# Kernel tuning notes

Measured on AMD Instinct MI355X. Metric: run time of the kernel, lower is better.

## Reference

```python
import jax, jax.numpy as jnp
import numpy as np

K = 9          # knn_num
EPS = 1e-5     # BatchNorm eps


def _conv2d(x, w, stride):
    # x: NCHW, w: OIHW, VALID padding
    return jax.lax.conv_general_dilated(
        x, w, window_strides=stride, padding='VALID',
        dimension_numbers=('NCHW', 'OIHW', 'NCHW'))


def _bn_relu(x, gamma, beta):
    # training-mode BatchNorm2d (biased batch stats over N,H,W) + ReLU
    mean = jnp.mean(x, axis=(0, 2, 3), keepdims=True)
    var = jnp.var(x, axis=(0, 2, 3), keepdims=True)
    xhat = (x - mean) * jax.lax.rsqrt(var + EPS)
    return jax.nn.relu(xhat * gamma[None, :, None, None] + beta[None, :, None, None])


def setup_inputs() -> dict:
    key = jax.random.key(0)
    ks = jax.random.split(key, 5)
    B, C, N = 16, 128, 2048
    features = jax.random.normal(ks[0], (B, C, N, 1), dtype=jnp.float32)
    fan1 = 2 * C * 1 * 3
    W1 = jax.random.normal(ks[1], (C, 2 * C, 1, 3), dtype=jnp.float32) / np.sqrt(fan1)
    b1 = jnp.zeros((C,), dtype=jnp.float32)
    g1 = jnp.ones((C,), dtype=jnp.float32)
    beta1 = jnp.zeros((C,), dtype=jnp.float32)
    fan2 = C * 1 * 3
    W2 = jax.random.normal(ks[2], (C, C, 1, 3), dtype=jnp.float32) / np.sqrt(fan2)
    b2 = jnp.zeros((C,), dtype=jnp.float32)
    g2 = jnp.ones((C,), dtype=jnp.float32)
    beta2 = jnp.zeros((C,), dtype=jnp.float32)
    return {"features": features, "W1": W1, "b1": b1, "g1": g1, "beta1": beta1,
            "W2": W2, "b2": b2, "g2": g2, "beta2": beta2}


def reference(features, W1, b1, g1, beta1, W2, b2, g2, beta2):
    B, C, N, _ = features.shape
    x = features.reshape(B, C, N)
    # pairwise_distance[b,i,j] = -||x_i||^2 + 2 x_i.x_j - ||x_j||^2 = -||x_i - x_j||^2
    xx = jnp.sum(x * x, axis=1)                      # (B, N)
    inner = jnp.einsum('bci,bcj->bij', x, x)          # (B, N, N)
    pd = 2.0 * inner - xx[:, :, None] - xx[:, None, :]
    _, idx = jax.lax.top_k(pd, K)                     # (B, N, K) nearest neighbors (incl. self)
    xT = jnp.transpose(x, (0, 2, 1))                  # (B, N, C)
    feature = xT[jnp.arange(B)[:, None, None], idx]   # (B, N, K, C) gathered neighbors
    xc = xT[:, :, None, :]                            # (B, N, 1, C)
    diff = xc - feature
    # torch: cat(x, (x - f) - |x - f|) along channel dim -> (B, N, K, 2C)
    edge = jnp.concatenate(
        [jnp.broadcast_to(xc, diff.shape), diff - jnp.abs(diff)], axis=3)
    edge = jnp.transpose(edge, (0, 3, 1, 2))          # (B, 2C, N, K)
    h = _conv2d(edge, W1, (1, 3)) + b1[None, :, None, None]   # (B, C, N, 3)
    h = _bn_relu(h, g1, beta1)
    h = _conv2d(h, W2, (1, 1)) + b2[None, :, None, None]       # (B, C, N, 1)
    h = _bn_relu(h, g2, beta2)
    return h
```

## Files before the change

### kernel.cpp

```cpp
#include <hip/hip_runtime.h>
#include <cstddef>

#define BATCH 16
#define CH    128
#define NPTS  2048
#define KNN   9

typedef const __attribute__((address_space(1))) void* gptr_t;
typedef __attribute__((address_space(3))) void* lptr_t;

__global__ void k_transpose(const float* __restrict__ x, float* __restrict__ xT) {
  __shared__ float tile[32][33];
  int b = blockIdx.z;
  int n0 = blockIdx.x * 32, c0 = blockIdx.y * 32;
  int tx = threadIdx.x, ty = threadIdx.y;
#pragma unroll
  for (int i = 0; i < 4; ++i) {
    int cc = c0 + ty + i * 8;
    tile[ty + i * 8][tx] = x[((size_t)b * CH + cc) * NPTS + n0 + tx];
  }
  __syncthreads();
#pragma unroll
  for (int i = 0; i < 4; ++i) {
    int nn = n0 + ty + i * 8;
    xT[((size_t)b * NPTS + nn) * CH + c0 + tx] = tile[tx][ty + i * 8];
  }
}

__global__ void k_xx_pw(const float* __restrict__ x, float* __restrict__ xx) {
  int g = blockIdx.x * 256 + threadIdx.x;
  int b = g >> 11, n = g & (NPTS - 1);
  const float* p = x + (size_t)b * CH * NPTS + n;
  float s[128];
#pragma unroll
  for (int c = 0; c < 128; ++c) {
    float v = p[(size_t)c * NPTS];
    s[c] = __fmul_rn(v, v);
  }
  float lane[16];
#pragma unroll
  for (int l = 0; l < 16; ++l) {
    lane[l] = __fadd_rn(
        __fadd_rn(__fadd_rn(s[l], s[16 + l]), __fadd_rn(s[32 + l], s[48 + l])),
        __fadd_rn(__fadd_rn(s[64 + l], s[80 + l]), __fadd_rn(s[96 + l], s[112 + l])));
  }
  float m8[8];
#pragma unroll
  for (int i = 0; i < 8; ++i) m8[i] = __fadd_rn(lane[i], lane[i + 8]);
  float n4[4];
#pragma unroll
  for (int i = 0; i < 4; ++i) n4[i] = __fadd_rn(m8[i], m8[i + 4]);
  float p2[2];
#pragma unroll
  for (int i = 0; i < 2; ++i) p2[i] = __fadd_rn(n4[i], n4[i + 2]);
  xx[g] = __fadd_rn(p2[0], p2[1]);
}

__global__ __launch_bounds__(256) void k_knn_np(const float* __restrict__ x,
                                                const float* __restrict__ xx,
                                                int* __restrict__ idxout) {
  __shared__ __align__(16) char smraw[65536];
  float (*rowT)[64] = (float (*)[64])smraw;
  float* colA = (float*)(smraw + 32768);
  float* colB = (float*)(smraw + 49152);
  float (*mv)[145] = (float (*)[145])smraw;
  unsigned short (*mi)[145] = (unsigned short (*)[145])(smraw + 37120);

  int b = blockIdx.y;
  int n0 = blockIdx.x * 64;
  int tid = threadIdx.x;
  int tx = tid & 15, ty = tid >> 4;

  const float* gb = x + (size_t)b * CH * NPTS;

#pragma unroll
  for (int i = 0; i < 8; ++i) {
    int e = i * 1024 + tid * 4;
    const float* ga = gb + (size_t)(e >> 6) * NPTS + n0 + (e & 63);
    __builtin_amdgcn_global_load_lds((gptr_t)ga, (lptr_t)(&rowT[0][0] + e), 16, 0, 0);
  }

  float tv[4][9];
  int   ti[4][9];
#pragma unroll
  for (int m = 0; m < 4; ++m)
#pragma unroll
    for (int s = 0; s < 9; ++s) { tv[m][s] = -3.4e38f; ti[m][s] = 0x7fffffff; }

  float xr[4];
#pragma unroll
  for (int m = 0; m < 4; ++m) xr[m] = xx[(size_t)b * NPTS + n0 + ty * 4 + m];

#pragma unroll
  for (int i = 0; i < 4; ++i) {
    int e = i * 1024 + tid * 4;
    const float* ga = gb + (size_t)(e >> 6) * NPTS + 0 + (e & 63);
    __builtin_amdgcn_global_load_lds((gptr_t)ga, (lptr_t)(colA + e), 16, 0, 0);
  }

  for (int jt = 0; jt < NPTS; jt += 64) {
    int jnext = (jt + 64) & (NPTS - 1);

    __builtin_amdgcn_s_barrier();
#pragma unroll
    for (int i = 0; i < 4; ++i) {
      int e = i * 1024 + tid * 4;
      const float* ga = gb + (size_t)(64 + (e >> 6)) * NPTS + jt + (e & 63);
      __builtin_amdgcn_global_load_lds((gptr_t)ga, (lptr_t)(colB + e), 16, 0, 0);
    }
    asm volatile("s_waitcnt vmcnt(4)" ::: "memory");
    __builtin_amdgcn_s_barrier();

    float acc[4][4];
#pragma unroll
    for (int m = 0; m < 4; ++m)
#pragma unroll
      for (int nn = 0; nn < 4; ++nn) acc[m][nn] = 0.f;

#pragma unroll 8
    for (int k2 = 0; k2 < 64; ++k2) {
      float a[4], bv[4];
      *(float4*)a  = *(const float4*)&rowT[k2][ty * 4];
      *(float4*)bv = *(const float4*)(colA + k2 * 64 + tx * 4);
#pragma unroll
      for (int m = 0; m < 4; ++m)
#pragma unroll
        for (int nn = 0; nn < 4; ++nn)
          acc[m][nn] = __builtin_fmaf(a[m], bv[nn], acc[m][nn]);
    }

    __builtin_amdgcn_s_barrier();
#pragma unroll
    for (int i = 0; i < 4; ++i) {
      int e = i * 1024 + tid * 4;
      const float* ga = gb + (size_t)(e >> 6) * NPTS + jnext + (e & 63);
      __builtin_amdgcn_global_load_lds((gptr_t)ga, (lptr_t)(colA + e), 16, 0, 0);
    }
    asm volatile("s_waitcnt vmcnt(4)" ::: "memory");
    __builtin_amdgcn_s_barrier();

#pragma unroll 8
    for (int k2 = 0; k2 < 64; ++k2) {
      float a[4], bv[4];
      *(float4*)a  = *(const float4*)&rowT[64 + k2][ty * 4];
      *(float4*)bv = *(const float4*)(colB + k2 * 64 + tx * 4);
#pragma unroll
      for (int m = 0; m < 4; ++m)
#pragma unroll
        for (int nn = 0; nn < 4; ++nn)
          acc[m][nn] = __builtin_fmaf(a[m], bv[nn], acc[m][nn]);
    }

#pragma unroll
    for (int nn = 0; nn < 4; ++nn) {
      int j = jt + tx * 4 + nn;
      float xc = xx[(size_t)b * NPTS + j];
#pragma unroll
      for (int m = 0; m < 4; ++m) {
        float val = __fsub_rn(__fsub_rn(__fmul_rn(2.0f, acc[m][nn]), xr[m]), xc);
        if (val > tv[m][8]) {
          float cv = val; int ci = j;
#pragma unroll
          for (int s = 0; s < 9; ++s) {
            bool sw = cv > tv[m][s];
            float t1 = tv[m][s]; int t2 = ti[m][s];
            tv[m][s] = sw ? cv : t1;  ti[m][s] = sw ? ci : t2;
            cv = sw ? t1 : cv;        ci = sw ? t2 : ci;
          }
        }
      }
    }
  }

  __syncthreads();
#pragma unroll
  for (int m = 0; m < 4; ++m) {
    int row = ty * 4 + m;
#pragma unroll
    for (int s = 0; s < 9; ++s) {
      mv[row][tx * 9 + s] = tv[m][s];
      mi[row][tx * 9 + s] = (unsigned short)ti[m][s];
    }
  }
  __syncthreads();
  if (tid < 64) {
    int row = tid;
    size_t base = ((size_t)b * NPTS + n0 + row) * KNN;
    for (int s = 0; s < KNN; ++s) {
      float best = -3.4e38f; int bj = 0x7fffffff; int bq = 0;
      for (int q = 0; q < 144; ++q) {
        float v = mv[row][q]; int jj = (int)mi[row][q];
        if (v > best || (v == best && jj < bj)) { best = v; bj = jj; bq = q; }
      }
      mv[row][bq] = -3.4e38f;
      idxout[base + s] = bj;
    }
  }
}

__global__ void k_prep(const float* __restrict__ W1, const float* __restrict__ W2,
                       float* __restrict__ At, float* __restrict__ W2t) {
  int g = blockIdx.x * 256 + threadIdx.x;
  if (g < 512 * 128) {
    int k = g / 128, o = g % 128;
    float v;
    if (k < 384) v = W1[(size_t)o * 768 + 384 + k];
    else {
      int c = k - 384;
      v = W1[(size_t)o * 768 + c * 3] + W1[(size_t)o * 768 + c * 3 + 1] +
          W1[(size_t)o * 768 + c * 3 + 2];
    }
    At[(size_t)k * 128 + o] = v;
  }
  if (g < 384 * 128) {
    int k = g / 128, o = g % 128;
    W2t[(size_t)k * 128 + o] = W2[(size_t)o * 384 + k];
  }
}

#define NN1 8
__global__ __launch_bounds__(256) void k_conv1(const float* __restrict__ xT,
                                               const int* __restrict__ knn_idx,
                                               const float* __restrict__ At,
                                               const float* __restrict__ bias1,
                                               float* __restrict__ h1) {
  __shared__ float dminL[NN1][KNN][132];
  __shared__ float xnL[NN1][132];
  __shared__ __align__(16) float AL[32][128];
  __shared__ int   idxL[NN1][KNN];
  int b = blockIdx.y;
  int n0 = blockIdx.x * NN1;
  int tid = threadIdx.x;

  if (tid < NN1 * KNN) {
    int n = tid / KNN, k = tid % KNN;
    idxL[n][k] = knn_idx[((size_t)b * NPTS + n0 + n) * KNN + k];
  }
  {
    int n = tid >> 5, q = tid & 31;
    float4 v = *(const float4*)&xT[((size_t)b * NPTS + n0 + n) * CH + q * 4];
    *(float4*)&xnL[n][q * 4] = v;
  }
  __syncthreads();
#pragma unroll
  for (int i = 0; i < 9; ++i) {
    int e = tid + i * 256;
    int rrow = e >> 5, q = e & 31;
    int n = rrow / KNN, k = rrow % KNN;
    int j = idxL[n][k];
    float4 xj = *(const float4*)&xT[((size_t)b * NPTS + j) * CH + q * 4];
    float4 xn = *(const float4*)&xnL[n][q * 4];
    float4 d;
    d.x = 2.0f * fminf(xn.x - xj.x, 0.0f);
    d.y = 2.0f * fminf(xn.y - xj.y, 0.0f);
    d.z = 2.0f * fminf(xn.z - xj.z, 0.0f);
    d.w = 2.0f * fminf(xn.w - xj.w, 0.0f);
    *(float4*)&dminL[n][k][q * 4] = d;
  }

  int n = tid & (NN1 - 1);
  int og = tid >> 3;
  float acc[4][3];
#pragma unroll
  for (int o = 0; o < 4; ++o)
#pragma unroll
    for (int t = 0; t < 3; ++t) acc[o][t] = 0.f;

  for (int kc = 0; kc < 16; ++kc) {
    __syncthreads();
#pragma unroll
    for (int i = 0; i < 3; ++i) {
      int e = i * 1024 + tid * 4;
      const float* ga = At + (size_t)kc * 3072 + e;
      __builtin_amdgcn_global_load_lds((gptr_t)ga, (lptr_t)(&AL[0][0] + e), 16, 0, 0);
    }
    asm volatile("s_waitcnt vmcnt(0)" ::: "memory");
    __syncthreads();

#pragma unroll
    for (int half = 0; half < 2; ++half) {
      int cbase = kc * 8 + half * 4;
      float q9[9][4];
#pragma unroll
      for (int nr = 0; nr < 9; ++nr)
        *(float4*)q9[nr] = *(const float4*)&dminL[n][nr][cbase];

#pragma unroll
      for (int kk = 0; kk < 12; ++kk) {
        int ci = kk / 3, r = kk % 3;
        float a[4];
        *(float4*)a = *(const float4*)&AL[half * 12 + kk][og * 4];
#pragma unroll
        for (int o = 0; o < 4; ++o) {
          acc[o][0] = fmaf(a[o], q9[r][ci],     acc[o][0]);
          acc[o][1] = fmaf(a[o], q9[3 + r][ci], acc[o][1]);
          acc[o][2] = fmaf(a[o], q9[6 + r][ci], acc[o][2]);
        }
      }
    }
  }

  for (int kc2 = 0; kc2 < 4; ++kc2) {
    __syncthreads();
#pragma unroll
    for (int i = 0; i < 4; ++i) {
      int e = i * 1024 + tid * 4;
      const float* ga = At + (size_t)(384 + kc2 * 32) * 128 + e;
      __builtin_amdgcn_global_load_lds((gptr_t)ga, (lptr_t)(&AL[0][0] + e), 16, 0, 0);
    }
    asm volatile("s_waitcnt vmcnt(0)" ::: "memory");
    __syncthreads();
#pragma unroll 4
    for (int kk = 0; kk < 32; ++kk) {
      int c = kc2 * 32 + kk;
      float a[4];
      *(float4*)a = *(const float4*)&AL[kk][og * 4];
      float b0 = xnL[n][c];
#pragma unroll
      for (int o = 0; o < 4; ++o) {
        acc[o][0] = fmaf(a[o], b0, acc[o][0]);
        acc[o][1] = fmaf(a[o], b0, acc[o][1]);
        acc[o][2] = fmaf(a[o], b0, acc[o][2]);
      }
    }
  }

#pragma unroll
  for (int o = 0; o < 4; ++o) {
    int oo = og * 4 + o;
    float bs = bias1[oo];
    size_t base = ((size_t)(b * CH + oo) * NPTS + n0 + n) * 3;
#pragma unroll
    for (int t = 0; t < 3; ++t) h1[base + t] = acc[o][t] + bs;
  }
}

__global__ void k_stats_partial(const float* __restrict__ src, double* __restrict__ psum,
                                double* __restrict__ psq, int slablen) {
  __shared__ double ls[256], lq[256];
  int blk = blockIdx.x;
  const float* p = src + (size_t)blk * slablen;
  double s = 0.0, q = 0.0;
  for (int i = threadIdx.x; i < slablen; i += 256) {
    double v = (double)p[i];
    s += v; q = fma(v, v, q);
  }
  ls[threadIdx.x] = s; lq[threadIdx.x] = q;
  __syncthreads();
  for (int off = 128; off > 0; off >>= 1) {
    if (threadIdx.x < off) {
      ls[threadIdx.x] += ls[threadIdx.x + off];
      lq[threadIdx.x] += lq[threadIdx.x + off];
    }
    __syncthreads();
  }
  if (threadIdx.x == 0) { psum[blk] = ls[0]; psq[blk] = lq[0]; }
}

__global__ void k_stats_final(const double* __restrict__ psum, const double* __restrict__ psq,
                              const float* __restrict__ gamma, const float* __restrict__ beta,
                              float* __restrict__ aout, float* __restrict__ cout_,
                              double inv_n) {
  int c = threadIdx.x;
  if (c < CH) {
    double s = 0.0, q = 0.0;
    for (int b = 0; b < BATCH; ++b) { s += psum[b * CH + c]; q += psq[b * CH + c]; }
    double mean = s * inv_n;
    double var = q * inv_n - mean * mean;
    double a = (double)gamma[c] / sqrt(var + 1e-5);
    aout[c] = (float)a;
    cout_[c] = (float)((double)beta[c] - mean * a);
  }
}

__global__ __launch_bounds__(256) void k_conv2(const float* __restrict__ h1,
                                               const float* __restrict__ W2t,
                                               const float* __restrict__ bias2,
                                               const float* __restrict__ a1,
                                               const float* __restrict__ c1,
                                               float* __restrict__ out) {
  __shared__ float actL[384][36];
  __shared__ __align__(16) float WL[16][128];
  int b = blockIdx.y, n0 = blockIdx.x * 32, tid = threadIdx.x;
#pragma unroll
  for (int i = 0; i < 12; ++i) {
    int e = tid + i * 256;
    int c = e / 24, q = e % 24;
    float4 v = *(const float4*)&h1[((size_t)(b * CH + c) * NPTS + n0) * 3 + q * 4];
    float aa = a1[c], cc = c1[c];
    float vv[4] = {v.x, v.y, v.z, v.w};
#pragma unroll
    for (int s = 0; s < 4; ++s) {
      int f = q * 4 + s;
      int nn = f / 3, t = f - nn * 3;
      actL[c * 3 + t][nn] = fmaxf(0.0f, fmaf(vv[s], aa, cc));
    }
  }
  int ng = tid & 7, og = tid >> 3;
  float acc[4][4];
#pragma unroll
  for (int o = 0; o < 4; ++o)
#pragma unroll
    for (int nn = 0; nn < 4; ++nn) acc[o][nn] = 0.f;

  for (int kc = 0; kc < 24; ++kc) {
    __syncthreads();
    {
      int e = tid * 4;
      const float* ga = W2t + (size_t)kc * 2048 + e;
      __builtin_amdgcn_global_load_lds((gptr_t)ga, (lptr_t)(&WL[0][0] + e), 16, 0, 0);
      ga += 1024;
      __builtin_amdgcn_global_load_lds((gptr_t)ga, (lptr_t)(&WL[0][0] + 1024 + e), 16, 0, 0);
    }
    asm volatile("s_waitcnt vmcnt(0)" ::: "memory");
    __syncthreads();
#pragma unroll 4
    for (int kk = 0; kk < 16; ++kk) {
      float a[4], bv[4];
      *(float4*)a  = *(const float4*)&WL[kk][og * 4];
      *(float4*)bv = *(const float4*)&actL[kc * 16 + kk][ng * 4];
#pragma unroll
      for (int o = 0; o < 4; ++o)
#pragma unroll
        for (int nn = 0; nn < 4; ++nn) acc[o][nn] = fmaf(a[o], bv[nn], acc[o][nn]);
    }
  }
#pragma unroll
  for (int o = 0; o < 4; ++o) {
    int oo = og * 4 + o;
    float bs = bias2[oo];
    size_t base = (size_t)(b * CH + oo) * NPTS + n0 + ng * 4;
#pragma unroll
    for (int nn = 0; nn < 4; ++nn) out[base + nn] = acc[o][nn] + bs;
  }
}

__global__ void k_bnrelu(float* __restrict__ out, const float* __restrict__ a2,
                         const float* __restrict__ c2) {
  int g = blockIdx.x * 256 + threadIdx.x;
  int c = (g >> 11) & 127;
  float v = out[g];
  out[g] = fmaxf(0.0f, fmaf(v, a2[c], c2[c]));
}

extern "C" void kernel_launch(void* const* d_in, const int* in_sizes, int n_in,
                              void* d_out, int out_size, void* d_ws, size_t ws_size,
                              hipStream_t stream) {
  const float* x   = (const float*)d_in[0];
  const float* W1  = (const float*)d_in[1];
  const float* b1  = (const float*)d_in[2];
  const float* g1  = (const float*)d_in[3];
  const float* be1 = (const float*)d_in[4];
  const float* W2  = (const float*)d_in[5];
  const float* b2  = (const float*)d_in[6];
  const float* g2  = (const float*)d_in[7];
  const float* be2 = (const float*)d_in[8];
  float* out = (float*)d_out;

  char* ws = (char*)d_ws;
  float*  xT      = (float*) (ws);
  float*  xx      = (float*) (ws + 16777216);
  int*    knn_idx = (int*)   (ws + 16908288);
  float*  At      = (float*) (ws + 18087936);
  float*  W2t     = (float*) (ws + 18350080);
  float*  h1      = (float*) (ws + 18546688);
  double* psum    = (double*)(ws + 68878336);
  double* psq     = (double*)(ws + 68894720);
  float*  a1      = (float*) (ws + 68911104);
  float*  c1      = (float*) (ws + 68911616);
  float*  a2      = (float*) (ws + 68912128);
  float*  c2      = (float*) (ws + 68912640);

  k_transpose<<<dim3(NPTS / 32, CH / 32, BATCH), dim3(32, 8), 0, stream>>>(x, xT);
  k_xx_pw<<<(BATCH * NPTS) / 256, 256, 0, stream>>>(x, xx);
  k_knn_np<<<dim3(NPTS / 64, BATCH), 256, 0, stream>>>(x, xx, knn_idx);
  k_prep<<<256, 256, 0, stream>>>(W1, W2, At, W2t);
  k_conv1<<<dim3(NPTS / NN1, BATCH), 256, 0, stream>>>(xT, knn_idx, At, b1, h1);
  k_stats_partial<<<BATCH * CH, 256, 0, stream>>>(h1, psum, psq, NPTS * 3);
  k_stats_final<<<1, 128, 0, stream>>>(psum, psq, g1, be1, a1, c1,
                                       1.0 / (double)(BATCH * NPTS * 3));
  k_conv2<<<dim3(NPTS / 32, BATCH), 256, 0, stream>>>(h1, W2t, b2, a1, c1, out);
  k_stats_partial<<<BATCH * CH, 256, 0, stream>>>(out, psum, psq, NPTS);
  k_stats_final<<<1, 128, 0, stream>>>(psum, psq, g2, be2, a2, c2,
                                       1.0 / (double)(BATCH * NPTS));
  k_bnrelu<<<(BATCH * CH * NPTS) / 256, 256, 0, stream>>>(out, a2, c2);
}
```

Measured before the change: 789.4 us.

## Double-buffer weight tiles in conv1 and conv2 with async LDS prefetch

Moves conv1 and conv2 shared memory to dynamic allocation and adds a second weight buffer, so the next K-chunk of weights is fetched with global_load_lds while the current chunk is being used. The full vmcnt(0) wait per iteration becomes a partial wait, and raw s_barrier replaces __syncthreads. The aim is to hide global weight-load latency behind the FMA loop. In exchange, LDS per block grows, which may lower occupancy on a kernel that was already heavy on LDS.

```diff
diff --git a/kernel.cpp b/kernel.cpp
--- a/kernel.cpp
+++ b/kernel.cpp
@@ -224,10 +224,11 @@
                                                const float* __restrict__ At,
                                                const float* __restrict__ bias1,
                                                float* __restrict__ h1) {
-  __shared__ float dminL[NN1][KNN][132];
-  __shared__ float xnL[NN1][132];
-  __shared__ __align__(16) float AL[32][128];
-  __shared__ int   idxL[NN1][KNN];
+  extern __shared__ __align__(16) char sm1[];
+  float (*dminL)[KNN][132] = (float (*)[KNN][132])sm1;
+  float (*xnL)[132] = (float (*)[132])(sm1 + 38016);
+  int   (*idxL)[KNN] = (int (*)[KNN])(sm1 + 42240);
+  float* ALb = (float*)(sm1 + 42528);
   int b = blockIdx.y;
   int n0 = blockIdx.x * NN1;
   int tid = threadIdx.x;
@@ -240,6 +241,11 @@
     int n = tid >> 5, q = tid & 31;
     float4 v = *(const float4*)&xT[((size_t)b * NPTS + n0 + n) * CH + q * 4];
     *(float4*)&xnL[n][q * 4] = v;
+  }
+#pragma unroll
+  for (int i = 0; i < 3; ++i) {
+    int e = i * 1024 + tid * 4;
+    __builtin_amdgcn_global_load_lds((gptr_t)(At + e), (lptr_t)(ALb + e), 16, 0, 0);
   }
   __syncthreads();
 #pragma unroll
@@ -257,6 +263,7 @@
     d.w = 2.0f * fminf(xn.w - xj.w, 0.0f);
     *(float4*)&dminL[n][k][q * 4] = d;
   }
+  __syncthreads();
 
   int n = tid & (NN1 - 1);
   int og = tid >> 3;
@@ -267,16 +274,21 @@
     for (int t = 0; t < 3; ++t) acc[o][t] = 0.f;
 
   for (int kc = 0; kc < 16; ++kc) {
-    __syncthreads();
-#pragma unroll
-    for (int i = 0; i < 3; ++i) {
-      int e = i * 1024 + tid * 4;
-      const float* ga = At + (size_t)kc * 3072 + e;
-      __builtin_amdgcn_global_load_lds((gptr_t)ga, (lptr_t)(&AL[0][0] + e), 16, 0, 0);
-    }
-    asm volatile("s_waitcnt vmcnt(0)" ::: "memory");
-    __syncthreads();
-
+    __builtin_amdgcn_s_barrier();
+    {
+      int knext = (kc + 1) & 15;
+      float* dst = ALb + ((kc + 1) & 1) * 3072;
+#pragma unroll
+      for (int i = 0; i < 3; ++i) {
+        int e = i * 1024 + tid * 4;
+        __builtin_amdgcn_global_load_lds((gptr_t)(At + (size_t)knext * 3072 + e),
+                                         (lptr_t)(dst + e), 16, 0, 0);
+      }
+    }
+    asm volatile("s_waitcnt vmcnt(3)" ::: "memory");
+    __builtin_amdgcn_s_barrier();
+
+    const float* AL = ALb + (kc & 1) * 3072;
 #pragma unroll
     for (int half = 0; half < 2; ++half) {
       int cbase = kc * 8 + half * 4;
@@ -289,7 +301,7 @@
       for (int kk = 0; kk < 12; ++kk) {
         int ci = kk / 3, r = kk % 3;
         float a[4];
-        *(float4*)a = *(const float4*)&AL[half * 12 + kk][og * 4];
+        *(float4*)a = *(const float4*)&AL[(half * 12 + kk) * 128 + og * 4];
 #pragma unroll
         for (int o = 0; o < 4; ++o) {
           acc[o][0] = fmaf(a[o], q9[r][ci],     acc[o][0]);
@@ -306,7 +318,7 @@
     for (int i = 0; i < 4; ++i) {
       int e = i * 1024 + tid * 4;
       const float* ga = At + (size_t)(384 + kc2 * 32) * 128 + e;
-      __builtin_amdgcn_global_load_lds((gptr_t)ga, (lptr_t)(&AL[0][0] + e), 16, 0, 0);
+      __builtin_amdgcn_global_load_lds((gptr_t)ga, (lptr_t)(ALb + e), 16, 0, 0);
     }
     asm volatile("s_waitcnt vmcnt(0)" ::: "memory");
     __syncthreads();
@@ -314,7 +326,7 @@
     for (int kk = 0; kk < 32; ++kk) {
       int c = kc2 * 32 + kk;
       float a[4];
-      *(float4*)a = *(const float4*)&AL[kk][og * 4];
+      *(float4*)a = *(const float4*)&ALb[kk * 128 + og * 4];
       float b0 = xnL[n][c];
 #pragma unroll
       for (int o = 0; o < 4; ++o) {
@@ -379,9 +391,16 @@
                                                const float* __restrict__ a1,
                                                const float* __restrict__ c1,
                                                float* __restrict__ out) {
-  __shared__ float actL[384][36];
-  __shared__ __align__(16) float WL[16][128];
+  extern __shared__ __align__(16) char sm2[];
+  float (*actL)[36] = (float (*)[36])sm2;
+  float* WLb = (float*)(sm2 + 55296);
   int b = blockIdx.y, n0 = blockIdx.x * 32, tid = threadIdx.x;
+
+  {
+    int e = tid * 4;
+    __builtin_amdgcn_global_load_lds((gptr_t)(W2t + e), (lptr_t)(WLb + e), 16, 0, 0);
+    __builtin_amdgcn_global_load_lds((gptr_t)(W2t + 1024 + e), (lptr_t)(WLb + 1024 + e), 16, 0, 0);
+  }
 #pragma unroll
   for (int i = 0; i < 12; ++i) {
     int e = tid + i * 256;
@@ -396,6 +415,8 @@
       actL[c * 3 + t][nn] = fmaxf(0.0f, fmaf(vv[s], aa, cc));
     }
   }
+  __syncthreads();
+
   int ng = tid & 7, og = tid >> 3;
   float acc[4][4];
 #pragma unroll
@@ -404,20 +425,24 @@
     for (int nn = 0; nn < 4; ++nn) acc[o][nn] = 0.f;
 
   for (int kc = 0; kc < 24; ++kc) {
-    __syncthreads();
+    __builtin_amdgcn_s_barrier();
     {
+      int knext = kc + 1 == 24 ? 23 : kc + 1;
+      float* dst = WLb + ((kc + 1) & 1) * 2048;
       int e = tid * 4;
-      const float* ga = W2t + (size_t)kc * 2048 + e;
-      __builtin_amdgcn_global_load_lds((gptr_t)ga, (lptr_t)(&WL[0][0] + e), 16, 0, 0);
-      ga += 1024;
-      __builtin_amdgcn_global_load_lds((gptr_t)ga, (lptr_t)(&WL[0][0] + 1024 + e), 16, 0, 0);
-    }
-    asm volatile("s_waitcnt vmcnt(0)" ::: "memory");
-    __syncthreads();
+      __builtin_amdgcn_global_load_lds((gptr_t)(W2t + (size_t)knext * 2048 + e),
+                                       (lptr_t)(dst + e), 16, 0, 0);
+      __builtin_amdgcn_global_load_lds((gptr_t)(W2t + (size_t)knext * 2048 + 1024 + e),
+                                       (lptr_t)(dst + 1024 + e), 16, 0, 0);
+    }
+    asm volatile("s_waitcnt vmcnt(2)" ::: "memory");
+    __builtin_amdgcn_s_barrier();
+
+    const float* WL = WLb + (kc & 1) * 2048;
 #pragma unroll 4
     for (int kk = 0; kk < 16; ++kk) {
       float a[4], bv[4];
-      *(float4*)a  = *(const float4*)&WL[kk][og * 4];
+      *(float4*)a  = *(const float4*)&WL[kk * 128 + og * 4];
       *(float4*)bv = *(const float4*)&actL[kc * 16 + kk][ng * 4];
 #pragma unroll
       for (int o = 0; o < 4; ++o)
@@ -425,6 +450,8 @@
         for (int nn = 0; nn < 4; ++nn) acc[o][nn] = fmaf(a[o], bv[nn], acc[o][nn]);
     }
   }
+  __syncthreads();
+
 #pragma unroll
   for (int o = 0; o < 4; ++o) {
     int oo = og * 4 + o;
@@ -471,15 +498,20 @@
   float*  a2      = (float*) (ws + 68912128);
   float*  c2      = (float*) (ws + 68912640);
 
+  (void)hipFuncSetAttribute((const void*)k_conv1,
+                            hipFuncAttributeMaxDynamicSharedMemorySize, 67104);
+  (void)hipFuncSetAttribute((const void*)k_conv2,
+                            hipFuncAttributeMaxDynamicSharedMemorySize, 71680);
+
   k_transpose<<<dim3(NPTS / 32, CH / 32, BATCH), dim3(32, 8), 0, stream>>>(x, xT);
   k_xx_pw<<<(BATCH * NPTS) / 256, 256, 0, stream>>>(x, xx);
   k_knn_np<<<dim3(NPTS / 64, BATCH), 256, 0, stream>>>(x, xx, knn_idx);
   k_prep<<<256, 256, 0, stream>>>(W1, W2, At, W2t);
-  k_conv1<<<dim3(NPTS / NN1, BATCH), 256, 0, stream>>>(xT, knn_idx, At, b1, h1);
+  k_conv1<<<dim3(NPTS / NN1, BATCH), 256, 67104, stream>>>(xT, knn_idx, At, b1, h1);
   k_stats_partial<<<BATCH * CH, 256, 0, stream>>>(h1, psum, psq, NPTS * 3);
   k_stats_final<<<1, 128, 0, stream>>>(psum, psq, g1, be1, a1, c1,
                                        1.0 / (double)(BATCH * NPTS * 3));
-  k_conv2<<<dim3(NPTS / 32, BATCH), 256, 0, stream>>>(h1, W2t, b2, a1, c1, out);
+  k_conv2<<<dim3(NPTS / 32, BATCH), 256, 71680, stream>>>(h1, W2t, b2, a1, c1, out);
   k_stats_partial<<<BATCH * CH, 256, 0, stream>>>(out, psum, psq, NPTS);
   k_stats_final<<<1, 128, 0, stream>>>(psum, psq, g2, be2, a2, c2,
                                        1.0 / (double)(BATCH * NPTS));
```

After: 811.9 us. +2.8%, slower.
